# Kernel optimization log

Hardware: AMD Instinct MI355X
Metric: run time of the kernel (lower is better)

The kernel has to match this reference:

```python
import jax, jax.numpy as jnp
import numpy as np

DIM = 1024
NUM_HEADS = 16
DIM_HEAD = 64
INNER = NUM_HEADS * DIM_HEAD  # 1024
B, N = 2, 2048


def setup_inputs() -> dict:
    key = jax.random.key(0)
    k1, k2, k3 = jax.random.split(key, 3)
    x = jax.random.normal(k1, (B, N, DIM), dtype=jnp.float32)
    # nn.Linear(dim, inner*3, bias=False): weight [3*inner, dim]; y = x @ W^T
    w_qkv = jax.random.normal(k2, (3 * INNER, DIM), dtype=jnp.float32) * (DIM ** -0.5)
    # to_out: Linear(inner, dim) with bias
    w_out = jax.random.normal(k3, (DIM, INNER), dtype=jnp.float32) * (INNER ** -0.5)
    b_out = jnp.zeros((DIM,), dtype=jnp.float32)
    return {"x": x, "w_qkv": w_qkv, "w_out": w_out, "b_out": b_out}


def reference(x, w_qkv, w_out, b_out):
    b, n, d = x.shape
    scale = DIM_HEAD ** -0.5
    qkv = jnp.einsum('bnd,ed->bne', x, w_qkv)  # [b, n, 3*inner]
    q, k, v = jnp.split(qkv, 3, axis=-1)
    # [b, n, h, dh] -> [b, h, n, dh]
    reshape = lambda t: t.reshape(b, n, NUM_HEADS, DIM_HEAD).transpose(0, 2, 1, 3)
    q, k, v = reshape(q), reshape(k), reshape(v)
    dots = jnp.einsum('bhqd,bhkd->bhqk', q, k) * scale  # [b, h, n, n]
    attn = jax.nn.softmax(dots, axis=-1)
    out = jnp.einsum('bhqk,bhkd->bhqd', attn, v)
    out = out.transpose(0, 2, 1, 3).reshape(b, n, INNER)
    out = jnp.einsum('bni,oi->bno', out, w_out) + b_out
    return out
```

## Files before the change

kernel.cpp:

```cpp
#include <hip/hip_runtime.h>
#include <hip/hip_bf16.h>
#include <stdint.h>

typedef unsigned short u16;
typedef short bf16x8 __attribute__((ext_vector_type(8)));
typedef float f32x4 __attribute__((ext_vector_type(4)));
typedef float f32x16 __attribute__((ext_vector_type(16)));
typedef u16 u16x4 __attribute__((ext_vector_type(4)));
typedef unsigned int uint2v __attribute__((ext_vector_type(2)));

#define DIMX  1024
#define NHEAD 16
#define DH    64
#define INNER 1024
#define BATCH 2
#define SEQ   2048
#define MTOT  (BATCH*SEQ)
#define EQKV  (3*INNER)

__device__ __forceinline__ u16 f2bf(float f) {
  unsigned int x = __float_as_uint(f);
  unsigned int r = (x + 0x7FFFu + ((x >> 16) & 1u)) >> 16;
  return (u16)r;
}

__device__ __forceinline__ unsigned int cvtpk(float lo, float hi) {
  unsigned int r;
  asm("v_cvt_pk_bf16_f32 %0, %1, %2" : "=v"(r) : "v"(lo), "v"(hi));
  return r;
}

__device__ __forceinline__ void plswap_u(unsigned int& x, unsigned int& y) {
  auto r = __builtin_amdgcn_permlane32_swap(x, y, false, false);
  x = r[0]; y = r[1];
}
__device__ __forceinline__ void plswap_f2(float v, float& a, float& b) {
  unsigned int x = __float_as_uint(v), y = __float_as_uint(v);
  auto r = __builtin_amdgcn_permlane32_swap(x, y, false, false);
  a = __uint_as_float(r[0]); b = __uint_as_float(r[1]);
}

__device__ __forceinline__ void async16(void* lds, const void* g) {
  __builtin_amdgcn_global_load_lds(
      (const __attribute__((address_space(1))) unsigned int*)g,
      (__attribute__((address_space(3))) unsigned int*)lds,
      16, 0, 0);
}

__device__ __forceinline__ int swz4(int r) { return (r ^ (r >> 2)) & 3; }

__global__ void cvt_kernel(const float* __restrict__ in, u16* __restrict__ out, int n4) {
  int i = blockIdx.x * blockDim.x + threadIdx.x;
  if (i < n4) {
    float4 v = ((const float4*)in)[i];
    u16x4 o;
    o[0] = f2bf(v.x); o[1] = f2bf(v.y); o[2] = f2bf(v.z); o[3] = f2bf(v.w);
    ((u16x4*)out)[i] = o;
  }
}

__global__ __launch_bounds__(256) void gemm_qkv(const u16* __restrict__ X, const u16* __restrict__ W,
                                                u16* __restrict__ Qo, u16* __restrict__ Ko,
                                                u16* __restrict__ Vt) {
  __shared__ short sAll[16384];
  short* sA = sAll;
  short* sB = sAll + 8192;
  const int tid = threadIdx.x;
  const int wv = tid >> 6, l = tid & 63;
  const int lo = l & 15, hi = l >> 4;
  const int wr = wv >> 1, wc = wv & 1;

  int lin = blockIdx.x;
  int wgid = (lin & 7) * 96 + (lin >> 3);
  const int bx = wgid / 32;
  const int by = wgid % 32;
  const int tn = bx * 128, tm = by * 128;

  f32x4 acc[4][4];
#pragma unroll
  for (int i = 0; i < 4; i++)
#pragma unroll
    for (int j = 0; j < 4; j++) acc[i][j] = (f32x4){0.f, 0.f, 0.f, 0.f};

  auto stage = [&](int buf, int kt) {
    int k0 = kt * 32;
    int off = buf * 4096;
#pragma unroll
    for (int c = 0; c < 2; c++) {
      int R0 = wv * 32 + c * 16;
      int r = R0 + (l >> 2);
      int sc = ((l & 3) ^ swz4(r)) * 8;
      async16(&sA[off + R0 * 32], &X[(size_t)(tm + r) * DIMX + k0 + sc]);
      async16(&sB[off + R0 * 32], &W[(size_t)(tn + r) * DIMX + k0 + sc]);
    }
  };

  stage(0, 0);
  __syncthreads();

  for (int kt = 0; kt < DIMX / 32; kt++) {
    const int buf = kt & 1;
    if (kt + 1 < DIMX / 32) stage(buf ^ 1, kt + 1);
    bf16x8 af[4], bf[4];
#pragma unroll
    for (int i = 0; i < 4; i++) {
      int r = wr * 64 + i * 16 + lo;
      af[i] = *(const bf16x8*)&sA[buf * 4096 + r * 32 + ((hi ^ swz4(r)) * 8)];
    }
#pragma unroll
    for (int j = 0; j < 4; j++) {
      int r = wc * 64 + j * 16 + lo;
      bf[j] = *(const bf16x8*)&sB[buf * 4096 + r * 32 + ((hi ^ swz4(r)) * 8)];
    }
#pragma unroll
    for (int i = 0; i < 4; i++)
#pragma unroll
      for (int j = 0; j < 4; j++)
        acc[i][j] = __builtin_amdgcn_mfma_f32_16x16x32_bf16(af[i], bf[j], acc[i][j], 0, 0, 0);
    __syncthreads();
  }

  const int cls = tn >> 10;
  const float scale = 0.125f * 1.44269504088896f;

  if (cls < 2) {
#pragma unroll
    for (int i = 0; i < 4; i++) {
      int mbase = tm + wr * 64 + i * 16 + hi * 4;
#pragma unroll
      for (int j = 0; j < 4; j++) {
        int e = tn + wc * 64 + j * 16 + lo;
        int e2 = e & 1023, h = e2 >> 6, d = e2 & 63;
#pragma unroll
        for (int r = 0; r < 4; r++) {
          int mm = mbase + r;
          int b = mm >> 11, n = mm & 2047;
          float v = acc[i][j][r];
          if (cls == 0)
            Qo[(((size_t)(b * NHEAD + h)) * SEQ + n) * DH + d] = f2bf(v * scale);
          else
            Ko[(((size_t)(b * NHEAD + h)) * SEQ + n) * DH + d] = f2bf(v);
        }
      }
    }
  } else {
#pragma unroll
    for (int i = 0; i < 4; i++) {
#pragma unroll
      for (int j = 0; j < 4; j++) {
        int e = wc * 64 + j * 16 + lo;
#pragma unroll
        for (int r = 0; r < 4; r++) {
          int n = wr * 64 + i * 16 + hi * 4 + r;
          sAll[e * 128 + (((n >> 3) ^ (e & 15)) * 8) + (n & 7)] = (short)f2bf(acc[i][j][r]);
        }
      }
    }
    __syncthreads();
    int er = tid >> 1, half = tid & 1;
    int e2 = tn + er - 2048;
    int h = e2 >> 6, d = e2 & 63;
    int b = tm >> 11, nb = tm & 2047;
    u16* dst = &Vt[(((size_t)(b * NHEAD + h)) * DH + d) * SEQ + nb + half * 64];
#pragma unroll
    for (int k = 0; k < 8; k++) {
      int phys = (half * 8 + k) ^ (er & 15);
      bf16x8 v = *(const bf16x8*)&sAll[er * 128 + phys * 8];
      *(bf16x8*)&dst[k * 8] = v;
    }
  }
}

__global__ __launch_bounds__(256) void attn_kernel(const u16* __restrict__ Q, const u16* __restrict__ Kd,
                                                   const u16* __restrict__ Vt, u16* __restrict__ O) {
  __shared__ short sK[2][64 * 64];
  __shared__ short sV[2][64 * 64];
  const int tid = threadIdx.x, wv = tid >> 6, l = tid & 63;
  const int l31 = l & 31, hi5 = l >> 5, l7 = l & 7;

  int lin = blockIdx.y * gridDim.x + blockIdx.x;
  int wgid = (lin & 7) * 64 + (lin >> 3);
  int bx = wgid & 15;
  int bh = wgid >> 4;

  const int qw = bx * 128 + wv * 32;
  const u16* Qb = Q + (size_t)bh * SEQ * DH;
  const u16* Kb = Kd + (size_t)bh * SEQ * DH;
  const u16* Vb = Vt + (size_t)bh * DH * SEQ;

  bf16x8 qf[4];
#pragma unroll
  for (int kd = 0; kd < 4; kd++)
    qf[kd] = *(const bf16x8*)&Qb[(size_t)(qw + l31) * DH + kd * 16 + hi5 * 8];

  f32x16 o0, o1;
#pragma unroll
  for (int r = 0; r < 16; r++) { o0[r] = 0.f; o1[r] = 0.f; }
  float mrun = -1e30f, lsum = 0.f;
  const float THR = 11.0f;

  auto stage = [&](int buf, int t) {
    int kv0 = t * 64;
#pragma unroll
    for (int c = 0; c < 2; c++) {
      int rbase = wv * 16 + c * 8;
      int gr = rbase + (l >> 3);
      int sc = ((l & 7) ^ (l >> 3)) * 8;
      async16(&sK[buf][rbase * 64], &Kb[(size_t)(kv0 + gr) * DH + sc]);
      async16(&sV[buf][rbase * 64], &Vb[(size_t)gr * SEQ + kv0 + sc]);
    }
  };

  stage(0, 0);
  __syncthreads();

  for (int t = 0; t < SEQ / 64; t++) {
    const int cur = t & 1;
    if (t + 1 < SEQ / 64) stage(cur ^ 1, t + 1);

    bf16x8 kf0[4], kf1[4], vf0[4], vf1[4];
#pragma unroll
    for (int kd = 0; kd < 4; kd++) {
      int c16 = ((kd * 2 + hi5) ^ l7) * 8;
      kf0[kd] = *(const bf16x8*)&sK[cur][l31 * 64 + c16];
      kf1[kd] = *(const bf16x8*)&sK[cur][(32 + l31) * 64 + c16];
      vf0[kd] = *(const bf16x8*)&sV[cur][l31 * 64 + c16];
      vf1[kd] = *(const bf16x8*)&sV[cur][(32 + l31) * 64 + c16];
    }

    f32x16 s0, s1;
#pragma unroll
    for (int r = 0; r < 16; r++) { s0[r] = 0.f; s1[r] = 0.f; }
    __builtin_amdgcn_s_setprio(1);
#pragma unroll
    for (int kd = 0; kd < 4; kd++) {
      s0 = __builtin_amdgcn_mfma_f32_32x32x16_bf16(kf0[kd], qf[kd], s0, 0, 0, 0);
      s1 = __builtin_amdgcn_mfma_f32_32x32x16_bf16(kf1[kd], qf[kd], s1, 0, 0, 0);
    }
    __builtin_amdgcn_s_setprio(0);

    float tr[16];
#pragma unroll
    for (int r = 0; r < 16; r++) tr[r] = fmaxf(s0[r], s1[r]);
#pragma unroll
    for (int st = 8; st > 0; st >>= 1)
#pragma unroll
      for (int r = 0; r < st; r++) tr[r] = fmaxf(tr[r], tr[r + st]);
    float mxa, mxb;
    plswap_f2(tr[0], mxa, mxb);
    float mx = fmaxf(mxa, mxb);

    if (!__all(mx <= mrun + THR)) {
      float mnew = fmaxf(mrun, mx);
      float alpha = __builtin_amdgcn_exp2f(mrun - mnew);
      mrun = mnew;
      lsum *= alpha;
      o0 *= alpha;
      o1 *= alpha;
    }

    float sm[16];
#pragma unroll
    for (int r = 0; r < 16; r++) {
      s0[r] = __builtin_amdgcn_exp2f(s0[r] - mrun);
      s1[r] = __builtin_amdgcn_exp2f(s1[r] - mrun);
      sm[r] = s0[r] + s1[r];
    }
#pragma unroll
    for (int st = 8; st > 0; st >>= 1)
#pragma unroll
      for (int r = 0; r < st; r++) sm[r] += sm[r + st];
    lsum += sm[0];

    bf16x8 pa[4];
#pragma unroll
    for (int ks = 0; ks < 4; ks++) {
      const int sft = (ks & 1) * 8;
      float e0 = (ks < 2) ? s0[sft + 0] : s1[sft + 0];
      float e1 = (ks < 2) ? s0[sft + 1] : s1[sft + 1];
      float e2 = (ks < 2) ? s0[sft + 2] : s1[sft + 2];
      float e3 = (ks < 2) ? s0[sft + 3] : s1[sft + 3];
      float e4 = (ks < 2) ? s0[sft + 4] : s1[sft + 4];
      float e5 = (ks < 2) ? s0[sft + 5] : s1[sft + 5];
      float e6 = (ks < 2) ? s0[sft + 6] : s1[sft + 6];
      float e7 = (ks < 2) ? s0[sft + 7] : s1[sft + 7];
      unsigned int w0 = cvtpk(e0, e1);
      unsigned int w1 = cvtpk(e2, e3);
      unsigned int w2 = cvtpk(e4, e5);
      unsigned int w3 = cvtpk(e6, e7);
      plswap_u(w0, w2);
      plswap_u(w1, w3);
      union { unsigned int w[4]; bf16x8 v; } u;
      u.w[0] = w0; u.w[1] = w1; u.w[2] = w2; u.w[3] = w3;
      pa[ks] = u.v;
    }

    __builtin_amdgcn_s_setprio(1);
#pragma unroll
    for (int ks = 0; ks < 4; ks++) {
      o0 = __builtin_amdgcn_mfma_f32_32x32x16_bf16(vf0[ks], pa[ks], o0, 0, 0, 0);
      o1 = __builtin_amdgcn_mfma_f32_32x32x16_bf16(vf1[ks], pa[ks], o1, 0, 0, 0);
    }
    __builtin_amdgcn_s_setprio(0);
    __syncthreads();
  }

  float la, lb;
  plswap_f2(lsum, la, lb);
  float inv = 1.0f / (la + lb);

  int b = bh >> 4, h = bh & 15;
  int q = qw + l31;
  size_t orow = ((size_t)(b * SEQ + q)) * INNER + h * 64;
#pragma unroll
  for (int half = 0; half < 2; half++) {
    const f32x16& oo = half ? o1 : o0;
#pragma unroll
    for (int g = 0; g < 4; g++) {
      uint2v pk2;
      pk2[0] = cvtpk(oo[g * 4 + 0] * inv, oo[g * 4 + 1] * inv);
      pk2[1] = cvtpk(oo[g * 4 + 2] * inv, oo[g * 4 + 3] * inv);
      int dv = half * 32 + g * 8 + 4 * hi5;
      *(uint2v*)&O[orow + dv] = pk2;
    }
  }
}

__global__ __launch_bounds__(256) void gemm_out(const u16* __restrict__ A, const u16* __restrict__ W,
                                                const float* __restrict__ bias, float* __restrict__ out) {
  __shared__ short sAll[16384];
  short* sA = sAll;
  short* sB = sAll + 8192;
  const int tid = threadIdx.x;
  const int wv = tid >> 6, l = tid & 63;
  const int lo = l & 15, hi = l >> 4;
  const int wr = wv >> 1, wc = wv & 1;

  int lin = blockIdx.x;
  int wgid = (lin & 7) * 32 + (lin >> 3);
  const int bx = wgid / 32;
  const int by = wgid % 32;
  const int tn = bx * 128, tm = by * 128;

  f32x4 acc[4][4];
#pragma unroll
  for (int i = 0; i < 4; i++)
#pragma unroll
    for (int j = 0; j < 4; j++) acc[i][j] = (f32x4){0.f, 0.f, 0.f, 0.f};

  auto stage = [&](int buf, int kt) {
    int k0 = kt * 32;
    int off = buf * 4096;
#pragma unroll
    for (int c = 0; c < 2; c++) {
      int R0 = wv * 32 + c * 16;
      int r = R0 + (l >> 2);
      int sc = ((l & 3) ^ swz4(r)) * 8;
      async16(&sA[off + R0 * 32], &A[(size_t)(tm + r) * INNER + k0 + sc]);
      async16(&sB[off + R0 * 32], &W[(size_t)(tn + r) * INNER + k0 + sc]);
    }
  };

  stage(0, 0);
  __syncthreads();

  for (int kt = 0; kt < INNER / 32; kt++) {
    const int buf = kt & 1;
    if (kt + 1 < INNER / 32) stage(buf ^ 1, kt + 1);
    bf16x8 af[4], bf[4];
#pragma unroll
    for (int i = 0; i < 4; i++) {
      int r = wr * 64 + i * 16 + lo;
      af[i] = *(const bf16x8*)&sA[buf * 4096 + r * 32 + ((hi ^ swz4(r)) * 8)];
    }
#pragma unroll
    for (int j = 0; j < 4; j++) {
      int r = wc * 64 + j * 16 + lo;
      bf[j] = *(const bf16x8*)&sB[buf * 4096 + r * 32 + ((hi ^ swz4(r)) * 8)];
    }
#pragma unroll
    for (int i = 0; i < 4; i++)
#pragma unroll
      for (int j = 0; j < 4; j++)
        acc[i][j] = __builtin_amdgcn_mfma_f32_16x16x32_bf16(af[i], bf[j], acc[i][j], 0, 0, 0);
    __syncthreads();
  }

#pragma unroll
  for (int i = 0; i < 4; i++) {
    int mbase = tm + wr * 64 + i * 16 + hi * 4;
#pragma unroll
    for (int j = 0; j < 4; j++) {
      int col = tn + wc * 64 + j * 16 + lo;
      float bv = bias[col];
#pragma unroll
      for (int r = 0; r < 4; r++)
        out[(size_t)(mbase + r) * DIMX + col] = acc[i][j][r] + bv;
    }
  }
}

extern "C" void kernel_launch(void* const* d_in, const int* in_sizes, int n_in,
                              void* d_out, int out_size, void* d_ws, size_t ws_size,
                              hipStream_t stream) {
  const float* x     = (const float*)d_in[0];
  const float* w_qkv = (const float*)d_in[1];
  const float* w_out = (const float*)d_in[2];
  const float* b_out = (const float*)d_in[3];

  char* ws = (char*)d_ws;
  u16* xb    = (u16*)(ws);
  u16* wqkvb = (u16*)(ws + (size_t)8  * (1<<20));
  u16* woutb = (u16*)(ws + (size_t)14 * (1<<20));
  u16* Qd    = (u16*)(ws + (size_t)16 * (1<<20));
  u16* Kdd   = (u16*)(ws + (size_t)24 * (1<<20));
  u16* Vtd   = (u16*)(ws + (size_t)32 * (1<<20));
  u16* Od    = (u16*)(ws + (size_t)40 * (1<<20));

  cvt_kernel<<<(MTOT * DIMX / 4 + 255) / 256, 256, 0, stream>>>(x, xb, MTOT * DIMX / 4);
  cvt_kernel<<<(EQKV * DIMX / 4 + 255) / 256, 256, 0, stream>>>(w_qkv, wqkvb, EQKV * DIMX / 4);
  cvt_kernel<<<(DIMX * INNER / 4 + 255) / 256, 256, 0, stream>>>(w_out, woutb, DIMX * INNER / 4);

  gemm_qkv<<<768, 256, 0, stream>>>(xb, wqkvb, Qd, Kdd, Vtd);
  attn_kernel<<<dim3(SEQ / 128, BATCH * NHEAD), 256, 0, stream>>>(Qd, Kdd, Vtd, Od);
  gemm_out<<<256, 256, 0, stream>>>(Od, woutb, b_out, (float*)d_out);
}
```

Before: 136.7 us.

## Split attention KV range in two halves and merge partials via LSE

Splits each attention workgroup's key/value loop into two halves run by separate workgroups (doubling the grid to 1024 blocks), writing partial outputs transposed plus log-sum-exp values, then adds a merge kernel that combines them with a sigmoid weight. This is meant to increase parallelism and occupancy across the CUs for a grid that was only 512 blocks. It costs extra global traffic for partial outputs, an extra kernel launch, and uncoalesced scalar transposed stores. It also removes the setprio hints around the MFMA sections. The partial outputs reuse workspace regions of the no-longer-needed bf16 input and weight buffers, which relies on those buffers being dead by the time attention runs.

```diff
diff --git a/kernel.cpp b/kernel.cpp
--- a/kernel.cpp
+++ b/kernel.cpp
@@ -172,16 +172,20 @@
 }
 
 __global__ __launch_bounds__(256) void attn_kernel(const u16* __restrict__ Q, const u16* __restrict__ Kd,
-                                                   const u16* __restrict__ Vt, u16* __restrict__ O) {
+                                                   const u16* __restrict__ Vt,
+                                                   u16* __restrict__ OpA, u16* __restrict__ OpB,
+                                                   float* __restrict__ LseA, float* __restrict__ LseB) {
   __shared__ short sK[2][64 * 64];
   __shared__ short sV[2][64 * 64];
   const int tid = threadIdx.x, wv = tid >> 6, l = tid & 63;
   const int l31 = l & 31, hi5 = l >> 5, l7 = l & 7;
 
   int lin = blockIdx.y * gridDim.x + blockIdx.x;
-  int wgid = (lin & 7) * 64 + (lin >> 3);
-  int bx = wgid & 15;
-  int bh = wgid >> 4;
+  int wgid = (lin & 7) * 128 + (lin >> 3);
+  int bh = wgid >> 5;
+  int rest = wgid & 31;
+  int bx = rest >> 1;
+  int half = rest & 1;
 
   const int qw = bx * 128 + wv * 32;
   const u16* Qb = Q + (size_t)bh * SEQ * DH;
@@ -211,12 +215,13 @@
     }
   };
 
-  stage(0, 0);
+  const int t0 = half * 16, t1 = t0 + 16;
+  stage(0, t0);
   __syncthreads();
 
-  for (int t = 0; t < SEQ / 64; t++) {
+  for (int t = t0; t < t1; t++) {
     const int cur = t & 1;
-    if (t + 1 < SEQ / 64) stage(cur ^ 1, t + 1);
+    if (t + 1 < t1) stage(cur ^ 1, t + 1);
 
     bf16x8 kf0[4], kf1[4], vf0[4], vf1[4];
 #pragma unroll
@@ -231,13 +236,11 @@
     f32x16 s0, s1;
 #pragma unroll
     for (int r = 0; r < 16; r++) { s0[r] = 0.f; s1[r] = 0.f; }
-    __builtin_amdgcn_s_setprio(1);
 #pragma unroll
     for (int kd = 0; kd < 4; kd++) {
       s0 = __builtin_amdgcn_mfma_f32_32x32x16_bf16(kf0[kd], qf[kd], s0, 0, 0, 0);
       s1 = __builtin_amdgcn_mfma_f32_32x32x16_bf16(kf1[kd], qf[kd], s1, 0, 0, 0);
     }
-    __builtin_amdgcn_s_setprio(0);
 
     float tr[16];
 #pragma unroll
@@ -295,34 +298,70 @@
       pa[ks] = u.v;
     }
 
-    __builtin_amdgcn_s_setprio(1);
 #pragma unroll
     for (int ks = 0; ks < 4; ks++) {
       o0 = __builtin_amdgcn_mfma_f32_32x32x16_bf16(vf0[ks], pa[ks], o0, 0, 0, 0);
       o1 = __builtin_amdgcn_mfma_f32_32x32x16_bf16(vf1[ks], pa[ks], o1, 0, 0, 0);
     }
-    __builtin_amdgcn_s_setprio(0);
     __syncthreads();
   }
 
   float la, lb;
   plswap_f2(lsum, la, lb);
-  float inv = 1.0f / (la + lb);
-
-  int b = bh >> 4, h = bh & 15;
+  float lt = la + lb;
+  float inv = 1.0f / lt;
+  float lse = mrun + __log2f(lt);
+
+  u16* Op = half ? OpB : OpA;
+  float* Lse = half ? LseB : LseA;
   int q = qw + l31;
-  size_t orow = ((size_t)(b * SEQ + q)) * INNER + h * 64;
-#pragma unroll
-  for (int half = 0; half < 2; half++) {
-    const f32x16& oo = half ? o1 : o0;
-#pragma unroll
-    for (int g = 0; g < 4; g++) {
-      uint2v pk2;
-      pk2[0] = cvtpk(oo[g * 4 + 0] * inv, oo[g * 4 + 1] * inv);
-      pk2[1] = cvtpk(oo[g * 4 + 2] * inv, oo[g * 4 + 3] * inv);
-      int dv = half * 32 + g * 8 + 4 * hi5;
-      *(uint2v*)&O[orow + dv] = pk2;
-    }
+  if (hi5 == 0) Lse[(size_t)bh * SEQ + q] = lse;
+
+  u16* Obase = Op + (size_t)bh * DH * SEQ;
+#pragma unroll
+  for (int r = 0; r < 16; r++) {
+    int dv = (r & 3) + 8 * (r >> 2) + 4 * hi5;
+    Obase[(size_t)dv * SEQ + q] = f2bf(o0[r] * inv);
+    Obase[(size_t)(dv + 32) * SEQ + q] = f2bf(o1[r] * inv);
+  }
+}
+
+__global__ __launch_bounds__(256) void merge_kernel(const u16* __restrict__ OpA, const u16* __restrict__ OpB,
+                                                    const float* __restrict__ LseA, const float* __restrict__ LseB,
+                                                    u16* __restrict__ O) {
+  __shared__ float lsA[64 * 65];
+  __shared__ float lsB[64 * 65];
+  const int tid = threadIdx.x;
+  const int bh = blockIdx.y, qc = blockIdx.x;
+  const int b = bh >> 4, h = bh & 15;
+
+#pragma unroll
+  for (int i = 0; i < 2; i++) {
+    int idx = tid + i * 256;
+    int dv = idx >> 3, q8 = (idx & 7) * 8;
+    size_t goff = (size_t)bh * DH * SEQ + (size_t)dv * SEQ + qc * 64 + q8;
+    bf16x8 va = *(const bf16x8*)&OpA[goff];
+    bf16x8 vb = *(const bf16x8*)&OpB[goff];
+#pragma unroll
+    for (int j = 0; j < 8; j++) {
+      lsA[dv * 65 + q8 + j] = __uint_as_float(((unsigned int)(u16)va[j]) << 16);
+      lsB[dv * 65 + q8 + j] = __uint_as_float(((unsigned int)(u16)vb[j]) << 16);
+    }
+  }
+  __syncthreads();
+
+  const int lane = tid & 63, w = tid >> 6;
+#pragma unroll
+  for (int i = 0; i < 16; i++) {
+    int ql = w * 16 + i;
+    int q = qc * 64 + ql;
+    float la = LseA[(size_t)bh * SEQ + q];
+    float lb = LseB[(size_t)bh * SEQ + q];
+    float sig = 1.0f / (1.0f + __builtin_amdgcn_exp2f(lb - la));
+    float va = lsA[lane * 65 + ql];
+    float vb = lsB[lane * 65 + ql];
+    float out = vb + (va - vb) * sig;
+    O[((size_t)(b * SEQ + q)) * INNER + h * 64 + lane] = f2bf(out);
   }
 }
 
@@ -371,7 +410,7 @@
 #pragma unroll
     for (int i = 0; i < 4; i++) {
       int r = wr * 64 + i * 16 + lo;
-      af[i] = *(const bf16x8*)&sA[buf * 4096 + r * 32 + ((hi ^ swz4(r)) * 8)];
+      af[i] = *(const bf16x8*)&sAll[buf * 4096 + r * 32 + ((hi ^ swz4(r)) * 8)];
     }
 #pragma unroll
     for (int j = 0; j < 4; j++) {
@@ -416,12 +455,17 @@
   u16* Kdd   = (u16*)(ws + (size_t)24 * (1<<20));
   u16* Vtd   = (u16*)(ws + (size_t)32 * (1<<20));
   u16* Od    = (u16*)(ws + (size_t)40 * (1<<20));
+  u16*   OpA  = (u16*)(ws);
+  u16*   OpB  = (u16*)(ws + (size_t)48 * (1<<20));
+  float* LseA = (float*)(ws + (size_t)8 * (1<<20));
+  float* LseB = (float*)(ws + (size_t)8 * (1<<20) + (1<<19));
 
   cvt_kernel<<<(MTOT * DIMX / 4 + 255) / 256, 256, 0, stream>>>(x, xb, MTOT * DIMX / 4);
   cvt_kernel<<<(EQKV * DIMX / 4 + 255) / 256, 256, 0, stream>>>(w_qkv, wqkvb, EQKV * DIMX / 4);
   cvt_kernel<<<(DIMX * INNER / 4 + 255) / 256, 256, 0, stream>>>(w_out, woutb, DIMX * INNER / 4);
 
   gemm_qkv<<<768, 256, 0, stream>>>(xb, wqkvb, Qd, Kdd, Vtd);
-  attn_kernel<<<dim3(SEQ / 128, BATCH * NHEAD), 256, 0, stream>>>(Qd, Kdd, Vtd, Od);
+  attn_kernel<<<dim3(SEQ / 128 * 2, BATCH * NHEAD), 256, 0, stream>>>(Qd, Kdd, Vtd, OpA, OpB, LseA, LseB);
+  merge_kernel<<<dim3(SEQ / 64, BATCH * NHEAD), 256, 0, stream>>>(OpA, OpB, LseA, LseB, Od);
   gemm_out<<<256, 256, 0, stream>>>(Od, woutb, b_out, (float*)d_out);
 }
```

Measured after the change: 141.0 us. +3.2%, slower.
